# Kernel optimization log

Measured on AMD Instinct MI355X. Metric: run time of the kernel, lower is better.

## Reference

```python
import jax, jax.numpy as jnp
import numpy as np
import math

K = 2
CAPACITY = -1
NEED_L_AUX = True


def topk_gating(logits, k=K, capacity=CAPACITY, need_l_aux=NEED_L_AUX):
    # logits: (T, P, E) tokens x prototypes x experts-per-prototype
    gates = jax.nn.softmax(logits.astype(jnp.float32), axis=-1).astype(logits.dtype)
    T, P, E = gates.shape
    cap = int(math.ceil(1.25 * T / E)) if capacity < 0 else capacity

    idx1 = jnp.argmax(gates, axis=-1)                      # (T, P)
    mask1 = jax.nn.one_hot(idx1, E, dtype=jnp.int32)       # (T, P, E)
    loc1 = jnp.cumsum(mask1, axis=0) - 1                   # position in expert queue
    if need_l_aux:
        me = jnp.mean(gates, axis=0)
        ce = jnp.mean(mask1.astype(jnp.float32), axis=0)
        l_aux = jnp.mean(me * ce)
    else:
        l_aux = jnp.zeros((), jnp.float32)
    mask1 = mask1 * (loc1 < cap)                           # drop over-capacity tokens
    loc1_s = jnp.sum(loc1 * mask1, axis=-1)                # (T, P)
    gates1_s = jnp.sum(gates * mask1, axis=-1)
    denom = gates1_s
    gates_s_list = [gates1_s]
    mask_list = [mask1]
    loc_s_list = [loc1_s]
    last_logits = logits
    last_mask = mask1
    prev_masks = mask1
    for _ in range(2, k + 1):
        last_logits = jnp.where(last_mask.astype(bool), -jnp.inf, last_logits)
        idx = jnp.argmax(last_logits, axis=-1)
        mask = jax.nn.one_hot(idx, E, dtype=jnp.int32)
        loc = jnp.cumsum(mask, axis=0) - 1 + jnp.sum(prev_masks, axis=0, keepdims=True)
        mask = mask * (loc < cap)
        last_mask = mask
        prev_masks = prev_masks + mask
        mask_list.append(mask)
        loc_s_list.append(jnp.sum(loc * mask, axis=-1))
        gs = jnp.sum(gates * mask, axis=-1)
        denom = denom + gs
        gates_s_list.append(gs)
    denom = jnp.maximum(denom, jnp.finfo(denom.dtype).eps)

    combine = jnp.zeros((T, P, E, cap), gates.dtype)
    for gs, mask, ls in zip(gates_s_list, mask_list, loc_s_list):
        g = (gs / denom)[..., None] * mask                  # (T, P, E)
        loc_sc = jax.nn.one_hot(ls, cap, dtype=gates.dtype)  # (T, P, cap)
        combine = combine + g[..., None] * loc_sc[:, :, None, :]
    dispatch_mask = combine.astype(bool)
    return l_aux.astype(logits.dtype), combine.astype(logits.dtype), dispatch_mask


def setup_inputs() -> dict:
    key = jax.random.key(0)
    k1, k2 = jax.random.split(key)
    inp = jax.random.normal(k1, (4096, 2048), dtype=jnp.float32)
    W = jax.random.normal(k2, (64, 2048), dtype=jnp.float32) / math.sqrt(2048.0)
    return {"input": inp, "W": W, "bs": 4096, "prototypes": 2}


def reference(input, W, bs, prototypes):
    logits = input @ W.T                                   # (T, num_experts_total)
    logits = logits.reshape(input.shape[0], prototypes, -1)  # (T, P, E)
    return topk_gating(logits, k=K, capacity=CAPACITY, need_l_aux=NEED_L_AUX)
```

## Files before the change

kernel.cpp:

```cpp
#include <hip/hip_runtime.h>
#include <cstdint>

#define T_TOK 4096
#define KDIM 2048
#define NE 64
#define NP 2
#define EE 32
#define CAP 160
#define NKC 8
#define KCHUNK 256
#define BLKR 128
#define COMB_ELEMS 41943040ull
#define OUT_ELEMS 83886081ull
#define PARTF 2097152ull
#define TOT4 20971520
#define NFB 4096
#define SMALLF 65536
#define PB_F 81788928

__global__ __launch_bounds__(256) void k_gemm(const float* __restrict__ x,
                                              const float* __restrict__ W,
                                              float* __restrict__ part) {
  __shared__ float xs[BLKR][36];
  __shared__ float wt[32][68];
  const int tid = threadIdx.x;
  const int rb = (int)blockIdx.x & 31;
  const int kc = (int)blockIdx.x >> 5;
  const int r0 = rb * BLKR;
  const int er = tid & 15;
  const int rg = tid >> 4;
  float acc[8][4];
#pragma unroll
  for (int i = 0; i < 8; ++i)
#pragma unroll
    for (int c = 0; c < 4; ++c) acc[i][c] = 0.f;
  float4 sx[4], sw[2];
  {
    const int kb = kc * KCHUNK;
#pragma unroll
    for (int q = 0; q < 4; ++q) {
      const int li = tid + q * 256, row = li >> 3, kq = (li & 7) * 4;
      sx[q] = *reinterpret_cast<const float4*>(&x[(size_t)(r0 + row) * KDIM + kb + kq]);
    }
#pragma unroll
    for (int q = 0; q < 2; ++q) {
      const int li = tid + q * 256, e = li >> 3, kq = (li & 7) * 4;
      sw[q] = *reinterpret_cast<const float4*>(&W[(size_t)e * KDIM + kb + kq]);
    }
  }
  for (int s = 0; s < 8; ++s) {
    __syncthreads();
#pragma unroll
    for (int q = 0; q < 4; ++q) {
      const int li = tid + q * 256, row = li >> 3, kq = (li & 7) * 4;
      *reinterpret_cast<float4*>(&xs[row][kq]) = sx[q];
    }
#pragma unroll
    for (int q = 0; q < 2; ++q) {
      const int li = tid + q * 256, e = li >> 3, kq = (li & 7) * 4;
      wt[kq][e] = sw[q].x; wt[kq + 1][e] = sw[q].y;
      wt[kq + 2][e] = sw[q].z; wt[kq + 3][e] = sw[q].w;
    }
    if (s < 7) {
      const int kb = kc * KCHUNK + (s + 1) * 32;
#pragma unroll
      for (int q = 0; q < 4; ++q) {
        const int li = tid + q * 256, row = li >> 3, kq = (li & 7) * 4;
        sx[q] = *reinterpret_cast<const float4*>(&x[(size_t)(r0 + row) * KDIM + kb + kq]);
      }
#pragma unroll
      for (int q = 0; q < 2; ++q) {
        const int li = tid + q * 256, e = li >> 3, kq = (li & 7) * 4;
        sw[q] = *reinterpret_cast<const float4*>(&W[(size_t)e * KDIM + kb + kq]);
      }
    }
    __syncthreads();
#pragma unroll
    for (int k4 = 0; k4 < 8; ++k4) {
      float4 wb[4];
#pragma unroll
      for (int j = 0; j < 4; ++j)
        wb[j] = *reinterpret_cast<const float4*>(&wt[k4 * 4 + j][er * 4]);
#pragma unroll
      for (int i = 0; i < 8; ++i) {
        const float4 xv = *reinterpret_cast<const float4*>(&xs[rg + 16 * i][k4 * 4]);
        acc[i][0] = fmaf(xv.w, wb[3].x, fmaf(xv.z, wb[2].x, fmaf(xv.y, wb[1].x, fmaf(xv.x, wb[0].x, acc[i][0]))));
        acc[i][1] = fmaf(xv.w, wb[3].y, fmaf(xv.z, wb[2].y, fmaf(xv.y, wb[1].y, fmaf(xv.x, wb[0].y, acc[i][1]))));
        acc[i][2] = fmaf(xv.w, wb[3].z, fmaf(xv.z, wb[2].z, fmaf(xv.y, wb[1].z, fmaf(xv.x, wb[0].z, acc[i][2]))));
        acc[i][3] = fmaf(xv.w, wb[3].w, fmaf(xv.z, wb[2].w, fmaf(xv.y, wb[1].w, fmaf(xv.x, wb[0].w, acc[i][3]))));
      }
    }
  }
#pragma unroll
  for (int i = 0; i < 8; ++i) {
    float4 v; v.x = acc[i][0]; v.y = acc[i][1]; v.z = acc[i][2]; v.w = acc[i][3];
    *reinterpret_cast<float4*>(
        &part[((size_t)kc * T_TOK + r0 + rg + 16 * i) * NE + er * 4]) = v;
  }
}

__global__ __launch_bounds__(256)
void k_fillsoft(const float* __restrict__ part, float2* __restrict__ g12,
                int* __restrict__ idxs, float* __restrict__ me_part,
                float* __restrict__ out,
                int s1lo, int s1hi, int s2lo, int s2hi, int fillLast) {
  __shared__ float lg[64][33];
  const int tid = threadIdx.x;
  if (blockIdx.x >= 128) {
    const int fb = (int)blockIdx.x - 128;
    float4* p4 = reinterpret_cast<float4*>(out);
    const float4 z4 = make_float4(0.f, 0.f, 0.f, 0.f);
    const int start = fb * 5120;
#pragma unroll
    for (int j = 0; j < 20; ++j) {
      const int i4 = start + tid + j * 256;
      if (i4 >= s1lo && i4 < s1hi) continue;
      if (i4 >= s2lo && i4 < s2hi) continue;
      p4[i4] = z4;
    }
    if (fillLast && fb == NFB - 1 && tid == 255) out[OUT_ELEMS - 1] = 0.f;
    return;
  }
  if (tid < 64) {
    const int R = (int)blockIdx.x * 64 + tid;
    const int t = R >> 1;
    const int p = R & 1;
    float v[32];
    const float* pr = part + (size_t)t * NE + p * EE;
#pragma unroll
    for (int e = 0; e < 32; e += 4) {
      const float4 s = *reinterpret_cast<const float4*>(pr + e);
      v[e] = s.x; v[e + 1] = s.y; v[e + 2] = s.z; v[e + 3] = s.w;
    }
    for (int kc = 1; kc < NKC; ++kc) {
      const float* prk = pr + (size_t)kc * T_TOK * NE;
#pragma unroll
      for (int e = 0; e < 32; e += 4) {
        const float4 s = *reinterpret_cast<const float4*>(prk + e);
        v[e] += s.x; v[e + 1] += s.y; v[e + 2] += s.z; v[e + 3] += s.w;
      }
    }
    float m = v[0];
#pragma unroll
    for (int e = 1; e < 32; ++e) m = fmaxf(m, v[e]);
    float sum = 0.f;
#pragma unroll
    for (int e = 0; e < 32; ++e) { v[e] = expf(v[e] - m); sum += v[e]; }
    const float inv = 1.0f / sum;
#pragma unroll
    for (int e = 0; e < 32; ++e) v[e] *= inv;
    float g1 = -1.f; int i1 = 0;
#pragma unroll
    for (int e = 0; e < 32; ++e) if (v[e] > g1) { g1 = v[e]; i1 = e; }
    float g2 = -1.f; int i2 = 0;
#pragma unroll
    for (int e = 0; e < 32; ++e) if (e != i1 && v[e] > g2) { g2 = v[e]; i2 = e; }
    g12[R] = make_float2(g1, g2);
    idxs[R] = i1 | (i2 << 8);
#pragma unroll
    for (int e = 0; e < 32; ++e) lg[tid][e] = v[e];
  }
  __syncthreads();
  if (tid < 64) {
    const int pp = tid >> 5, ee = tid & 31;
    float s = 0.f;
    for (int rr = pp; rr < 64; rr += 2) s += lg[rr][ee];
    me_part[(int)blockIdx.x * 64 + tid] = s;
  }
}

__global__ __launch_bounds__(1024) void k_scan2(const int* __restrict__ idxs,
                                                const float2* __restrict__ g12,
                                                const float* __restrict__ me_part,
                                                int2* __restrict__ fl,
                                                float2* __restrict__ wvp,
                                                float* __restrict__ out,
                                                int rlimit) {
  __shared__ int grp[NP][64][32];
  __shared__ int tot[NP][32];
  __shared__ unsigned short tk1[NP][T_TOK];
  __shared__ unsigned short tk2[NP][T_TOK];
  __shared__ float red[64];
  const int tid = threadIdx.x;
  const int wvi = tid >> 6;
  const int p = wvi >> 3;
  const int wg = wvi & 7;
  const int l = tid & 63;
  const unsigned long long lmask = (1ull << l) - 1ull;
  for (int gi = 0; gi < 8; ++gi) {
    const int g = wg * 8 + gi;
    const int t = g * 64 + l;
    const int e1 = idxs[t * 2 + p] & 255;
    if (l < 32) grp[p][g][l] = 0;
    unsigned long long m = ~0ull;
#pragma unroll
    for (int b = 0; b < 5; ++b) {
      const unsigned long long bm = __ballot((e1 >> b) & 1);
      m &= ((e1 >> b) & 1) ? bm : ~bm;
    }
    const int rank = (int)__popcll(m & lmask);
    if (rank == 0) grp[p][g][e1] = (int)__popcll(m);
    tk1[p][t] = (unsigned short)(rank | (e1 << 6));
  }
  __syncthreads();
  if (tid < 64) {
    const int pp = tid >> 5, ee = tid & 31;
    int s = 0;
    for (int g = 0; g < 64; ++g) { int vv = grp[pp][g][ee]; grp[pp][g][ee] = s; s += vv; }
    tot[pp][ee] = s;
  }
  __syncthreads();
  for (int gi = 0; gi < 8; ++gi) {
    const int g = wg * 8 + gi;
    const int t = g * 64 + l;
    const int vv = tk1[p][t];
    tk1[p][t] = (unsigned short)(grp[p][g][vv >> 6] + (vv & 63));
  }
  if (tid < 64) {
    float s = 0.f;
    for (int b = 0; b < 128; ++b) s += me_part[b * 64 + tid];
    red[tid] = s * (float)tot[tid >> 5][tid & 31];
  }
  __syncthreads();
  if (tid == 0) {
    float s = 0.f;
    for (int i = 0; i < 64; ++i) s += red[i];
    out[0] = s / (64.0f * 4096.0f * 4096.0f);
  }
  for (int gi = 0; gi < 8; ++gi) {
    const int g = wg * 8 + gi;
    const int t = g * 64 + l;
    const int ii = idxs[t * 2 + p];
    const int e2 = (tk1[p][t] < CAP) ? (ii >> 8) : (ii & 255);
    if (l < 32) grp[p][g][l] = 0;
    unsigned long long m = ~0ull;
#pragma unroll
    for (int b = 0; b < 5; ++b) {
      const unsigned long long bm = __ballot((e2 >> b) & 1);
      m &= ((e2 >> b) & 1) ? bm : ~bm;
    }
    const int rank = (int)__popcll(m & lmask);
    if (rank == 0) grp[p][g][e2] = (int)__popcll(m);
    tk2[p][t] = (unsigned short)(rank | (e2 << 6));
  }
  __syncthreads();
  if (tid < 64) {
    const int pp = tid >> 5, ee = tid & 31;
    int s = min(tot[pp][ee], CAP);
    for (int g = 0; g < 64; ++g) { int vv = grp[pp][g][ee]; grp[pp][g][ee] = s; s += vv; }
  }
  __syncthreads();
  for (int gi = 0; gi < 8; ++gi) {
    const int g = wg * 8 + gi;
    const int t = g * 64 + l;
    const int R = t * 2 + p;
    const int ii = idxs[R];
    const int e1 = ii & 255;
    const int loc1v = tk1[p][t];
    const bool kept1 = loc1v < CAP;
    const int v2 = tk2[p][t];
    const int rank2 = v2 & 63, e2 = v2 >> 6;
    const int loc2 = grp[p][g][e2] + rank2;
    const bool kept2 = loc2 < CAP;
    const float2 gg = g12[R];
    const float gs1 = kept1 ? gg.x : 0.f;
    const float g2v = kept1 ? gg.y : gg.x;
    const float gs2 = kept2 ? g2v : 0.f;
    const float den = fmaxf(gs1 + gs2, 1.1920929e-07f);
    const int f1 = kept1 ? e1 * CAP + loc1v : -1;
    const int f2 = kept2 ? e2 * CAP + loc2 : -1;
    const float w1 = gs1 / den, w2 = gs2 / den;
    fl[R] = make_int2(f1, f2);
    wvp[R] = make_float2(w1, w2);
    float* oc = out + 1 + (size_t)R * 5120;
    if (f1 >= 0) oc[f1] = w1;
    if (f2 >= 0) oc[f2] = w2;
    if (R < rlimit) {
      float* od = out + 1 + COMB_ELEMS + (size_t)R * 5120;
      if (f1 >= 0) od[f1] = 1.0f;
      if (f2 >= 0) od[f2] = 1.0f;
    }
  }
}

__global__ __launch_bounds__(256) void k_tailB(float* __restrict__ out) {
  float4* p4 = reinterpret_cast<float4*>(out);
  const float4 z4 = make_float4(0.f, 0.f, 0.f, 0.f);
  const int base = 20447232 + (int)blockIdx.x * 4096 + (int)threadIdx.x;
#pragma unroll
  for (int j = 0; j < 16; ++j) p4[base + j * 256] = z4;
  if (blockIdx.x == 0 && threadIdx.x == 0) out[OUT_ELEMS - 1] = 0.f;
}

__global__ __launch_bounds__(256) void k_fill2C(float* __restrict__ out) {
  float4* p4 = reinterpret_cast<float4*>(out + 4);
  const float4 z4 = make_float4(0.f, 0.f, 0.f, 0.f);
  const int base = (int)blockIdx.x * 2048 + (int)threadIdx.x;
#pragma unroll
  for (int j = 0; j < 8; ++j) p4[base + j * 256] = z4;
}

__global__ __launch_bounds__(1024) void k_tailC(const int2* __restrict__ fl,
                                                float* __restrict__ out,
                                                int nfullB) {
  __shared__ int2 sfl[16];
  const int tid = threadIdx.x;
  const int rstart = nfullB * 2;
  const int nr = 8192 - rstart;
  if (tid < nr) sfl[tid] = fl[rstart + tid];
  __syncthreads();
  const size_t base = 1 + COMB_ELEMS + (size_t)rstart * 5120;
  const int cnt = nr * 5120;
  const int nx4 = (cnt - 4) >> 2;
  float4* p4 = (float4*)(out + base + 3);
  const float4 z4 = make_float4(0.f, 0.f, 0.f, 0.f);
  for (int idx = tid; idx < nx4; idx += 1024) p4[idx] = z4;
  if (tid < 3) out[base + tid] = 0.f;
  if (tid == 3) out[base + cnt - 1] = 0.f;
  __syncthreads();
  if (tid < 2 * nr) {
    const int rr = rstart + (tid >> 1);
    const int2 f = sfl[tid >> 1];
    const int pos = (tid & 1) ? f.y : f.x;
    if (pos >= 0) out[1 + COMB_ELEMS + (size_t)rr * 5120 + pos] = 1.0f;
  }
}

extern "C" void kernel_launch(void* const* d_in, const int* in_sizes, int n_in,
                              void* d_out, int out_size, void* d_ws, size_t ws_size,
                              hipStream_t stream) {
  const float* x = (const float*)d_in[0];
  const float* W = (const float*)d_in[1];
  float* out = (float*)d_out;

  const bool pathA = ws_size >= (SMALLF + PARTF) * sizeof(float);
  const bool pathB = !pathA && ws_size >= SMALLF * sizeof(float);

  float* small;
  float* part;
  int s1lo = 0, s1hi = 0, s2lo = 0, s2hi = 0, fillLast = 1;
  int rlimit = 8192, nfullB = 4096;
  if (pathA) {
    small = (float*)d_ws;
    part = small + SMALLF;
  } else if (pathB) {
    small = (float*)d_ws;
    part = out + PB_F;
    s1lo = PB_F / 4; s1hi = TOT4;
    fillLast = 0;
  } else {
    const size_t tb = (OUT_ELEMS - SMALLF) & ~(size_t)3;
    small = out + tb;
    part = out + 4;
    s1lo = 1; s1hi = 1 + (int)(PARTF / 4);
    s2lo = (int)(tb / 4); s2hi = TOT4;
    fillLast = 0;
    nfullB = (int)((tb - 1 - COMB_ELEMS) / 10240);
    rlimit = nfullB * 2;
  }
  float2* g12 = (float2*)small;
  int* idxs = (int*)(small + 16384);
  float* me_part = small + 24576;
  int2* fl = (int2*)(small + 32768);
  float2* wvp = (float2*)(small + 49152);

  hipLaunchKernelGGL(k_gemm, dim3(256), dim3(256), 0, stream, x, W, part);
  hipLaunchKernelGGL(k_fillsoft, dim3(128 + NFB), dim3(256), 0, stream,
                     part, g12, idxs, me_part, out, s1lo, s1hi, s2lo, s2hi, fillLast);
  if (pathB)
    hipLaunchKernelGGL(k_tailB, dim3(128), dim3(256), 0, stream, out);
  if (!pathA && !pathB)
    hipLaunchKernelGGL(k_fill2C, dim3(256), dim3(256), 0, stream, out);
  hipLaunchKernelGGL(k_scan2, dim3(1), dim3(1024), 0, stream,
                     idxs, g12, me_part, fl, wvp, out, rlimit);
  if (!pathA && !pathB)
    hipLaunchKernelGGL(k_tailC, dim3(1), dim3(1024), 0, stream, fl, out, nfullB);
}
```

Baseline: 124.5 us.

## Overlap output zero-fill with split-K GEMM in one fused kernel launch

The zero-fill blocks for the large combine output move out of the softmax kernel and into the GEMM launch, so the bandwidth-bound fill runs alongside the compute-bound GEMM blocks. The GEMM blocks grow to 512 threads with half the rows per thread, and the softmax becomes its own small 64-thread kernel. The aim is to hide the fill's memory traffic behind the GEMM and drop idle threads from the softmax blocks. The cost is fewer accumulators per thread and possible contention between the fill and GEMM blocks for bandwidth and CU slots.

```diff
diff --git a/kernel.cpp b/kernel.cpp
--- a/kernel.cpp
+++ b/kernel.cpp
@@ -9,70 +9,75 @@
 #define CAP 160
 #define NKC 8
 #define KCHUNK 256
-#define BLKR 128
 #define COMB_ELEMS 41943040ull
 #define OUT_ELEMS 83886081ull
 #define PARTF 2097152ull
 #define TOT4 20971520
-#define NFB 4096
 #define SMALLF 65536
 #define PB_F 81788928
 
-__global__ __launch_bounds__(256) void k_gemm(const float* __restrict__ x,
-                                              const float* __restrict__ W,
-                                              float* __restrict__ part) {
-  __shared__ float xs[BLKR][36];
+__global__ __launch_bounds__(512)
+void k_fused(const float* __restrict__ x, const float* __restrict__ W,
+             float* __restrict__ part, float* __restrict__ out,
+             int s1lo, int s1hi, int s2lo, int s2hi, int fillLast) {
+  __shared__ float xs[128][36];
   __shared__ float wt[32][68];
   const int tid = threadIdx.x;
+  if (blockIdx.x >= 256) {
+    const int fb = (int)blockIdx.x - 256;
+    float4* p4 = reinterpret_cast<float4*>(out);
+    const float4 z4 = make_float4(0.f, 0.f, 0.f, 0.f);
+    const int start = fb * 10240;
+#pragma unroll
+    for (int j = 0; j < 20; ++j) {
+      const int i4 = start + tid + j * 512;
+      if (i4 >= s1lo && i4 < s1hi) continue;
+      if (i4 >= s2lo && i4 < s2hi) continue;
+      p4[i4] = z4;
+    }
+    if (fillLast && fb == 2047 && tid == 511) out[OUT_ELEMS - 1] = 0.f;
+    return;
+  }
   const int rb = (int)blockIdx.x & 31;
   const int kc = (int)blockIdx.x >> 5;
-  const int r0 = rb * BLKR;
+  const int r0 = rb * 128;
   const int er = tid & 15;
   const int rg = tid >> 4;
-  float acc[8][4];
-#pragma unroll
-  for (int i = 0; i < 8; ++i)
+  float acc[4][4];
+#pragma unroll
+  for (int i = 0; i < 4; ++i)
 #pragma unroll
     for (int c = 0; c < 4; ++c) acc[i][c] = 0.f;
-  float4 sx[4], sw[2];
+  float4 sx[2], sw1;
   {
     const int kb = kc * KCHUNK;
 #pragma unroll
-    for (int q = 0; q < 4; ++q) {
-      const int li = tid + q * 256, row = li >> 3, kq = (li & 7) * 4;
+    for (int q = 0; q < 2; ++q) {
+      const int li = tid + q * 512, row = li >> 3, kq = (li & 7) * 4;
       sx[q] = *reinterpret_cast<const float4*>(&x[(size_t)(r0 + row) * KDIM + kb + kq]);
     }
-#pragma unroll
-    for (int q = 0; q < 2; ++q) {
-      const int li = tid + q * 256, e = li >> 3, kq = (li & 7) * 4;
-      sw[q] = *reinterpret_cast<const float4*>(&W[(size_t)e * KDIM + kb + kq]);
-    }
+    { const int e = tid >> 3, kq = (tid & 7) * 4;
+      sw1 = *reinterpret_cast<const float4*>(&W[(size_t)e * KDIM + kb + kq]); }
   }
   for (int s = 0; s < 8; ++s) {
     __syncthreads();
 #pragma unroll
-    for (int q = 0; q < 4; ++q) {
-      const int li = tid + q * 256, row = li >> 3, kq = (li & 7) * 4;
+    for (int q = 0; q < 2; ++q) {
+      const int li = tid + q * 512, row = li >> 3, kq = (li & 7) * 4;
       *reinterpret_cast<float4*>(&xs[row][kq]) = sx[q];
     }
-#pragma unroll
-    for (int q = 0; q < 2; ++q) {
-      const int li = tid + q * 256, e = li >> 3, kq = (li & 7) * 4;
-      wt[kq][e] = sw[q].x; wt[kq + 1][e] = sw[q].y;
-      wt[kq + 2][e] = sw[q].z; wt[kq + 3][e] = sw[q].w;
-    }
+    { const int e = tid >> 3, kq = (tid & 7) * 4;
+      wt[kq][e] = sw1.x; wt[kq + 1][e] = sw1.y;
+      wt[kq + 2][e] = sw1.z; wt[kq + 3][e] = sw1.w; }
     if (s < 7) {
       const int kb = kc * KCHUNK + (s + 1) * 32;
 #pragma unroll
-      for (int q = 0; q < 4; ++q) {
-        const int li = tid + q * 256, row = li >> 3, kq = (li & 7) * 4;
+      for (int q = 0; q < 2; ++q) {
+        const int li = tid + q * 512, row = li >> 3, kq = (li & 7) * 4;
         sx[q] = *reinterpret_cast<const float4*>(&x[(size_t)(r0 + row) * KDIM + kb + kq]);
       }
-#pragma unroll
-      for (int q = 0; q < 2; ++q) {
-        const int li = tid + q * 256, e = li >> 3, kq = (li & 7) * 4;
-        sw[q] = *reinterpret_cast<const float4*>(&W[(size_t)e * KDIM + kb + kq]);
-      }
+      { const int e = tid >> 3, kq = (tid & 7) * 4;
+        sw1 = *reinterpret_cast<const float4*>(&W[(size_t)e * KDIM + kb + kq]); }
     }
     __syncthreads();
 #pragma unroll
@@ -82,8 +87,8 @@
       for (int j = 0; j < 4; ++j)
         wb[j] = *reinterpret_cast<const float4*>(&wt[k4 * 4 + j][er * 4]);
 #pragma unroll
-      for (int i = 0; i < 8; ++i) {
-        const float4 xv = *reinterpret_cast<const float4*>(&xs[rg + 16 * i][k4 * 4]);
+      for (int i = 0; i < 4; ++i) {
+        const float4 xv = *reinterpret_cast<const float4*>(&xs[rg + 32 * i][k4 * 4]);
         acc[i][0] = fmaf(xv.w, wb[3].x, fmaf(xv.z, wb[2].x, fmaf(xv.y, wb[1].x, fmaf(xv.x, wb[0].x, acc[i][0]))));
         acc[i][1] = fmaf(xv.w, wb[3].y, fmaf(xv.z, wb[2].y, fmaf(xv.y, wb[1].y, fmaf(xv.x, wb[0].y, acc[i][1]))));
         acc[i][2] = fmaf(xv.w, wb[3].z, fmaf(xv.z, wb[2].z, fmaf(xv.y, wb[1].z, fmaf(xv.x, wb[0].z, acc[i][2]))));
@@ -92,80 +97,62 @@
     }
   }
 #pragma unroll
-  for (int i = 0; i < 8; ++i) {
+  for (int i = 0; i < 4; ++i) {
     float4 v; v.x = acc[i][0]; v.y = acc[i][1]; v.z = acc[i][2]; v.w = acc[i][3];
     *reinterpret_cast<float4*>(
-        &part[((size_t)kc * T_TOK + r0 + rg + 16 * i) * NE + er * 4]) = v;
-  }
-}
-
-__global__ __launch_bounds__(256)
-void k_fillsoft(const float* __restrict__ part, float2* __restrict__ g12,
-                int* __restrict__ idxs, float* __restrict__ me_part,
-                float* __restrict__ out,
-                int s1lo, int s1hi, int s2lo, int s2hi, int fillLast) {
+        &part[((size_t)kc * T_TOK + r0 + rg + 32 * i) * NE + er * 4]) = v;
+  }
+}
+
+__global__ __launch_bounds__(64) void k_soft(const float* __restrict__ part,
+                                             float2* __restrict__ g12,
+                                             int* __restrict__ idxs,
+                                             float* __restrict__ me_part) {
   __shared__ float lg[64][33];
   const int tid = threadIdx.x;
-  if (blockIdx.x >= 128) {
-    const int fb = (int)blockIdx.x - 128;
-    float4* p4 = reinterpret_cast<float4*>(out);
-    const float4 z4 = make_float4(0.f, 0.f, 0.f, 0.f);
-    const int start = fb * 5120;
-#pragma unroll
-    for (int j = 0; j < 20; ++j) {
-      const int i4 = start + tid + j * 256;
-      if (i4 >= s1lo && i4 < s1hi) continue;
-      if (i4 >= s2lo && i4 < s2hi) continue;
-      p4[i4] = z4;
-    }
-    if (fillLast && fb == NFB - 1 && tid == 255) out[OUT_ELEMS - 1] = 0.f;
-    return;
-  }
-  if (tid < 64) {
-    const int R = (int)blockIdx.x * 64 + tid;
-    const int t = R >> 1;
-    const int p = R & 1;
-    float v[32];
-    const float* pr = part + (size_t)t * NE + p * EE;
+  const int R = blockIdx.x * 64 + tid;
+  const int t = R >> 1;
+  const int p = R & 1;
+  float v[32];
+  const float* pr = part + (size_t)t * NE + p * EE;
+#pragma unroll
+  for (int e = 0; e < 32; e += 4) {
+    float4 s = *reinterpret_cast<const float4*>(pr + e);
+    v[e] = s.x; v[e + 1] = s.y; v[e + 2] = s.z; v[e + 3] = s.w;
+  }
+  for (int kc = 1; kc < NKC; ++kc) {
+    const float* prk = pr + (size_t)kc * T_TOK * NE;
 #pragma unroll
     for (int e = 0; e < 32; e += 4) {
-      const float4 s = *reinterpret_cast<const float4*>(pr + e);
-      v[e] = s.x; v[e + 1] = s.y; v[e + 2] = s.z; v[e + 3] = s.w;
-    }
-    for (int kc = 1; kc < NKC; ++kc) {
-      const float* prk = pr + (size_t)kc * T_TOK * NE;
-#pragma unroll
-      for (int e = 0; e < 32; e += 4) {
-        const float4 s = *reinterpret_cast<const float4*>(prk + e);
-        v[e] += s.x; v[e + 1] += s.y; v[e + 2] += s.z; v[e + 3] += s.w;
-      }
-    }
-    float m = v[0];
-#pragma unroll
-    for (int e = 1; e < 32; ++e) m = fmaxf(m, v[e]);
-    float sum = 0.f;
-#pragma unroll
-    for (int e = 0; e < 32; ++e) { v[e] = expf(v[e] - m); sum += v[e]; }
-    const float inv = 1.0f / sum;
-#pragma unroll
-    for (int e = 0; e < 32; ++e) v[e] *= inv;
-    float g1 = -1.f; int i1 = 0;
-#pragma unroll
-    for (int e = 0; e < 32; ++e) if (v[e] > g1) { g1 = v[e]; i1 = e; }
-    float g2 = -1.f; int i2 = 0;
-#pragma unroll
-    for (int e = 0; e < 32; ++e) if (e != i1 && v[e] > g2) { g2 = v[e]; i2 = e; }
-    g12[R] = make_float2(g1, g2);
-    idxs[R] = i1 | (i2 << 8);
-#pragma unroll
-    for (int e = 0; e < 32; ++e) lg[tid][e] = v[e];
-  }
-  __syncthreads();
-  if (tid < 64) {
+      float4 s = *reinterpret_cast<const float4*>(prk + e);
+      v[e] += s.x; v[e + 1] += s.y; v[e + 2] += s.z; v[e + 3] += s.w;
+    }
+  }
+  float m = v[0];
+#pragma unroll
+  for (int e = 1; e < 32; ++e) m = fmaxf(m, v[e]);
+  float sum = 0.f;
+#pragma unroll
+  for (int e = 0; e < 32; ++e) { v[e] = expf(v[e] - m); sum += v[e]; }
+  const float inv = 1.0f / sum;
+#pragma unroll
+  for (int e = 0; e < 32; ++e) v[e] *= inv;
+  float g1 = -1.f; int i1 = 0;
+#pragma unroll
+  for (int e = 0; e < 32; ++e) if (v[e] > g1) { g1 = v[e]; i1 = e; }
+  float g2 = -1.f; int i2 = 0;
+#pragma unroll
+  for (int e = 0; e < 32; ++e) if (e != i1 && v[e] > g2) { g2 = v[e]; i2 = e; }
+  g12[R] = make_float2(g1, g2);
+  idxs[R] = i1 | (i2 << 8);
+#pragma unroll
+  for (int e = 0; e < 32; ++e) lg[tid][e] = v[e];
+  __syncthreads();
+  {
     const int pp = tid >> 5, ee = tid & 31;
     float s = 0.f;
     for (int rr = pp; rr < 64; rr += 2) s += lg[rr][ee];
-    me_part[(int)blockIdx.x * 64 + tid] = s;
+    me_part[blockIdx.x * 64 + tid] = s;
   }
 }
 
@@ -364,9 +351,9 @@
   int2* fl = (int2*)(small + 32768);
   float2* wvp = (float2*)(small + 49152);
 
-  hipLaunchKernelGGL(k_gemm, dim3(256), dim3(256), 0, stream, x, W, part);
-  hipLaunchKernelGGL(k_fillsoft, dim3(128 + NFB), dim3(256), 0, stream,
-                     part, g12, idxs, me_part, out, s1lo, s1hi, s2lo, s2hi, fillLast);
+  hipLaunchKernelGGL(k_fused, dim3(2304), dim3(512), 0, stream,
+                     x, W, part, out, s1lo, s1hi, s2lo, s2hi, fillLast);
+  hipLaunchKernelGGL(k_soft, dim3(128), dim3(64), 0, stream, part, g12, idxs, me_part);
   if (pathB)
     hipLaunchKernelGGL(k_tailB, dim3(128), dim3(256), 0, stream, out);
   if (!pathA && !pathB)
```

Result: faster. 114.6 us (-7.9%).

## Spread output zero-fill across GEMM, softmax and scan kernels to overlap

Applied to the files above, without the earlier changes.

The 4096 zero-fill spans of the large output were all done in the softmax kernel. They are now split into three parts that run as extra blocks inside the GEMM launch, the softmax launch and the single-block scan launch. This hides the memory-bound fill behind the compute-light GEMM and the serial scan. Softmax now uses all 256 threads per block (32 blocks) instead of 64 active threads. The scatter of combine and dispatch values moves to a new small k_fix kernel that runs after every fill block has finished. The cost is one more launch and a fragile hand-tuned split of fill blocks across the kernels.

```diff
diff --git a/kernel.cpp b/kernel.cpp
--- a/kernel.cpp
+++ b/kernel.cpp
@@ -14,16 +14,40 @@
 #define OUT_ELEMS 83886081ull
 #define PARTF 2097152ull
 #define TOT4 20971520
-#define NFB 4096
 #define SMALLF 65536
 #define PB_F 81788928
-
-__global__ __launch_bounds__(256) void k_gemm(const float* __restrict__ x,
-                                              const float* __restrict__ W,
-                                              float* __restrict__ part) {
+#define NFA 3300
+#define NFB 450
+#define NFC 346
+
+template <int NTH, int ITERS>
+__device__ __forceinline__ void fill_span(float* __restrict__ out, int span, int tid,
+                                          int s1lo, int s1hi, int s2lo, int s2hi,
+                                          int fillLast) {
+  float4* p4 = reinterpret_cast<float4*>(out);
+  const float4 z4 = make_float4(0.f, 0.f, 0.f, 0.f);
+  const int start = span * 5120;
+#pragma unroll
+  for (int j = 0; j < ITERS; ++j) {
+    const int i4 = start + tid + j * NTH;
+    if (i4 >= s1lo && i4 < s1hi) continue;
+    if (i4 >= s2lo && i4 < s2hi) continue;
+    p4[i4] = z4;
+  }
+  if (fillLast && span == 4095 && tid == NTH - 1) out[OUT_ELEMS - 1] = 0.f;
+}
+
+__global__ __launch_bounds__(256)
+void k_fused(const float* __restrict__ x, const float* __restrict__ W,
+             float* __restrict__ part, float* __restrict__ out,
+             int s1lo, int s1hi, int s2lo, int s2hi) {
   __shared__ float xs[BLKR][36];
   __shared__ float wt[32][68];
   const int tid = threadIdx.x;
+  if (blockIdx.x >= 256) {
+    fill_span<256, 20>(out, (int)blockIdx.x - 256, tid, s1lo, s1hi, s2lo, s2hi, 0);
+    return;
+  }
   const int rb = (int)blockIdx.x & 31;
   const int kc = (int)blockIdx.x >> 5;
   const int r0 = rb * BLKR;
@@ -100,88 +124,79 @@
 }
 
 __global__ __launch_bounds__(256)
-void k_fillsoft(const float* __restrict__ part, float2* __restrict__ g12,
-                int* __restrict__ idxs, float* __restrict__ me_part,
-                float* __restrict__ out,
-                int s1lo, int s1hi, int s2lo, int s2hi, int fillLast) {
-  __shared__ float lg[64][33];
+void k_soft2(const float* __restrict__ part, float2* __restrict__ g12,
+             int* __restrict__ idxs, float* __restrict__ me_part,
+             float* __restrict__ out,
+             int s1lo, int s1hi, int s2lo, int s2hi) {
+  __shared__ float lg[256][33];
   const int tid = threadIdx.x;
-  if (blockIdx.x >= 128) {
-    const int fb = (int)blockIdx.x - 128;
-    float4* p4 = reinterpret_cast<float4*>(out);
-    const float4 z4 = make_float4(0.f, 0.f, 0.f, 0.f);
-    const int start = fb * 5120;
-#pragma unroll
-    for (int j = 0; j < 20; ++j) {
-      const int i4 = start + tid + j * 256;
-      if (i4 >= s1lo && i4 < s1hi) continue;
-      if (i4 >= s2lo && i4 < s2hi) continue;
-      p4[i4] = z4;
-    }
-    if (fillLast && fb == NFB - 1 && tid == 255) out[OUT_ELEMS - 1] = 0.f;
+  if (blockIdx.x >= 32) {
+    fill_span<256, 20>(out, NFA + (int)blockIdx.x - 32, tid, s1lo, s1hi, s2lo, s2hi, 0);
     return;
   }
-  if (tid < 64) {
-    const int R = (int)blockIdx.x * 64 + tid;
-    const int t = R >> 1;
-    const int p = R & 1;
-    float v[32];
-    const float* pr = part + (size_t)t * NE + p * EE;
+  const int R = (int)blockIdx.x * 256 + tid;
+  const int t = R >> 1;
+  const int p = R & 1;
+  float v[32];
+  const float* pr = part + (size_t)t * NE + p * EE;
+#pragma unroll
+  for (int e = 0; e < 32; e += 4) {
+    float4 s = *reinterpret_cast<const float4*>(pr + e);
+    v[e] = s.x; v[e + 1] = s.y; v[e + 2] = s.z; v[e + 3] = s.w;
+  }
+  for (int kc = 1; kc < NKC; ++kc) {
+    const float* prk = pr + (size_t)kc * T_TOK * NE;
 #pragma unroll
     for (int e = 0; e < 32; e += 4) {
-      const float4 s = *reinterpret_cast<const float4*>(pr + e);
-      v[e] = s.x; v[e + 1] = s.y; v[e + 2] = s.z; v[e + 3] = s.w;
-    }
-    for (int kc = 1; kc < NKC; ++kc) {
-      const float* prk = pr + (size_t)kc * T_TOK * NE;
-#pragma unroll
-      for (int e = 0; e < 32; e += 4) {
-        const float4 s = *reinterpret_cast<const float4*>(prk + e);
-        v[e] += s.x; v[e + 1] += s.y; v[e + 2] += s.z; v[e + 3] += s.w;
-      }
-    }
-    float m = v[0];
-#pragma unroll
-    for (int e = 1; e < 32; ++e) m = fmaxf(m, v[e]);
-    float sum = 0.f;
-#pragma unroll
-    for (int e = 0; e < 32; ++e) { v[e] = expf(v[e] - m); sum += v[e]; }
-    const float inv = 1.0f / sum;
-#pragma unroll
-    for (int e = 0; e < 32; ++e) v[e] *= inv;
-    float g1 = -1.f; int i1 = 0;
-#pragma unroll
-    for (int e = 0; e < 32; ++e) if (v[e] > g1) { g1 = v[e]; i1 = e; }
-    float g2 = -1.f; int i2 = 0;
-#pragma unroll
-    for (int e = 0; e < 32; ++e) if (e != i1 && v[e] > g2) { g2 = v[e]; i2 = e; }
-    g12[R] = make_float2(g1, g2);
-    idxs[R] = i1 | (i2 << 8);
-#pragma unroll
-    for (int e = 0; e < 32; ++e) lg[tid][e] = v[e];
-  }
-  __syncthreads();
-  if (tid < 64) {
-    const int pp = tid >> 5, ee = tid & 31;
+      float4 s = *reinterpret_cast<const float4*>(prk + e);
+      v[e] += s.x; v[e + 1] += s.y; v[e + 2] += s.z; v[e + 3] += s.w;
+    }
+  }
+  float m = v[0];
+#pragma unroll
+  for (int e = 1; e < 32; ++e) m = fmaxf(m, v[e]);
+  float sum = 0.f;
+#pragma unroll
+  for (int e = 0; e < 32; ++e) { v[e] = expf(v[e] - m); sum += v[e]; }
+  const float inv = 1.0f / sum;
+#pragma unroll
+  for (int e = 0; e < 32; ++e) v[e] *= inv;
+  float g1 = -1.f; int i1 = 0;
+#pragma unroll
+  for (int e = 0; e < 32; ++e) if (v[e] > g1) { g1 = v[e]; i1 = e; }
+  float g2 = -1.f; int i2 = 0;
+#pragma unroll
+  for (int e = 0; e < 32; ++e) if (e != i1 && v[e] > g2) { g2 = v[e]; i2 = e; }
+  g12[R] = make_float2(g1, g2);
+  idxs[R] = i1 | (i2 << 8);
+#pragma unroll
+  for (int e = 0; e < 32; ++e) lg[tid][e] = v[e];
+  __syncthreads();
+  {
+    const int wbase = (tid >> 6) * 64;
+    const int pp = (tid & 63) >> 5, ee = tid & 31;
     float s = 0.f;
-    for (int rr = pp; rr < 64; rr += 2) s += lg[rr][ee];
-    me_part[(int)blockIdx.x * 64 + tid] = s;
-  }
-}
-
-__global__ __launch_bounds__(1024) void k_scan2(const int* __restrict__ idxs,
-                                                const float2* __restrict__ g12,
-                                                const float* __restrict__ me_part,
-                                                int2* __restrict__ fl,
-                                                float2* __restrict__ wvp,
-                                                float* __restrict__ out,
-                                                int rlimit) {
+    for (int rr = pp; rr < 64; rr += 2) s += lg[wbase + rr][ee];
+    me_part[(int)blockIdx.x * 256 + tid] = s;
+  }
+}
+
+__global__ __launch_bounds__(1024)
+void k_scanf(const int* __restrict__ idxs, const float2* __restrict__ g12,
+             const float* __restrict__ me_part, int2* __restrict__ fl,
+             float2* __restrict__ wvp, float* __restrict__ out,
+             int s1lo, int s1hi, int s2lo, int s2hi, int fillLast) {
+  const int tid = threadIdx.x;
+  if (blockIdx.x >= 1) {
+    fill_span<1024, 5>(out, NFA + NFB + (int)blockIdx.x - 1, tid,
+                       s1lo, s1hi, s2lo, s2hi, fillLast);
+    return;
+  }
   __shared__ int grp[NP][64][32];
   __shared__ int tot[NP][32];
   __shared__ unsigned short tk1[NP][T_TOK];
   __shared__ unsigned short tk2[NP][T_TOK];
   __shared__ float red[64];
-  const int tid = threadIdx.x;
   const int wvi = tid >> 6;
   const int p = wvi >> 3;
   const int wg = wvi & 7;
@@ -267,19 +282,25 @@
     const float g2v = kept1 ? gg.y : gg.x;
     const float gs2 = kept2 ? g2v : 0.f;
     const float den = fmaxf(gs1 + gs2, 1.1920929e-07f);
-    const int f1 = kept1 ? e1 * CAP + loc1v : -1;
-    const int f2 = kept2 ? e2 * CAP + loc2 : -1;
-    const float w1 = gs1 / den, w2 = gs2 / den;
-    fl[R] = make_int2(f1, f2);
-    wvp[R] = make_float2(w1, w2);
-    float* oc = out + 1 + (size_t)R * 5120;
-    if (f1 >= 0) oc[f1] = w1;
-    if (f2 >= 0) oc[f2] = w2;
-    if (R < rlimit) {
-      float* od = out + 1 + COMB_ELEMS + (size_t)R * 5120;
-      if (f1 >= 0) od[f1] = 1.0f;
-      if (f2 >= 0) od[f2] = 1.0f;
-    }
+    fl[R] = make_int2(kept1 ? e1 * CAP + loc1v : -1, kept2 ? e2 * CAP + loc2 : -1);
+    wvp[R] = make_float2(gs1 / den, gs2 / den);
+  }
+}
+
+__global__ __launch_bounds__(256) void k_fix(const int2* __restrict__ fl,
+                                             const float2* __restrict__ wvp,
+                                             float* __restrict__ out,
+                                             int rlimit) {
+  const int R = (int)blockIdx.x * 256 + threadIdx.x;
+  const int2 f = fl[R];
+  const float2 w = wvp[R];
+  float* oc = out + 1 + (size_t)R * 5120;
+  if (f.x >= 0) oc[f.x] = w.x;
+  if (f.y >= 0) oc[f.y] = w.y;
+  if (R < rlimit) {
+    float* od = out + 1 + COMB_ELEMS + (size_t)R * 5120;
+    if (f.x >= 0) od[f.x] = 1.0f;
+    if (f.y >= 0) od[f.y] = 1.0f;
   }
 }
 
@@ -302,10 +323,9 @@
 
 __global__ __launch_bounds__(1024) void k_tailC(const int2* __restrict__ fl,
                                                 float* __restrict__ out,
-                                                int nfullB) {
+                                                int rstart) {
   __shared__ int2 sfl[16];
   const int tid = threadIdx.x;
-  const int rstart = nfullB * 2;
   const int nr = 8192 - rstart;
   if (tid < nr) sfl[tid] = fl[rstart + tid];
   __syncthreads();
@@ -339,7 +359,7 @@
   float* small;
   float* part;
   int s1lo = 0, s1hi = 0, s2lo = 0, s2hi = 0, fillLast = 1;
-  int rlimit = 8192, nfullB = 4096;
+  int rlimit = 8192, rstart = 8192;
   if (pathA) {
     small = (float*)d_ws;
     part = small + SMALLF;
@@ -355,8 +375,8 @@
     s1lo = 1; s1hi = 1 + (int)(PARTF / 4);
     s2lo = (int)(tb / 4); s2hi = TOT4;
     fillLast = 0;
-    nfullB = (int)((tb - 1 - COMB_ELEMS) / 10240);
-    rlimit = nfullB * 2;
+    rstart = (int)((tb - 1 - COMB_ELEMS) / 5120);
+    rlimit = rstart;
   }
   float2* g12 = (float2*)small;
   int* idxs = (int*)(small + 16384);
@@ -364,15 +384,17 @@
   int2* fl = (int2*)(small + 32768);
   float2* wvp = (float2*)(small + 49152);
 
-  hipLaunchKernelGGL(k_gemm, dim3(256), dim3(256), 0, stream, x, W, part);
-  hipLaunchKernelGGL(k_fillsoft, dim3(128 + NFB), dim3(256), 0, stream,
-                     part, g12, idxs, me_part, out, s1lo, s1hi, s2lo, s2hi, fillLast);
+  hipLaunchKernelGGL(k_fused, dim3(256 + NFA), dim3(256), 0, stream,
+                     x, W, part, out, s1lo, s1hi, s2lo, s2hi);
+  hipLaunchKernelGGL(k_soft2, dim3(32 + NFB), dim3(256), 0, stream,
+                     part, g12, idxs, me_part, out, s1lo, s1hi, s2lo, s2hi);
   if (pathB)
     hipLaunchKernelGGL(k_tailB, dim3(128), dim3(256), 0, stream, out);
   if (!pathA && !pathB)
     hipLaunchKernelGGL(k_fill2C, dim3(256), dim3(256), 0, stream, out);
-  hipLaunchKernelGGL(k_scan2, dim3(1), dim3(1024), 0, stream,
-                     idxs, g12, me_part, fl, wvp, out, rlimit);
+  hipLaunchKernelGGL(k_scanf, dim3(1 + NFC), dim3(1024), 0, stream,
+                     idxs, g12, me_part, fl, wvp, out, s1lo, s1hi, s2lo, s2hi, fillLast);
+  hipLaunchKernelGGL(k_fix, dim3(32), dim3(256), 0, stream, fl, wvp, out, rlimit);
   if (!pathA && !pathB)
-    hipLaunchKernelGGL(k_tailC, dim3(1), dim3(1024), 0, stream, fl, out, nfullB);
-}
+    hipLaunchKernelGGL(k_tailC, dim3(1), dim3(1024), 0, stream, fl, out, rstart);
+}
```

Result: faster. 108.6 us (-12.8%).
